# Kernel tuning notes

Measured on AMD Instinct MI355X. Metric: run time of the kernel, lower is better.

Reference implementation:

```python
import jax, jax.numpy as jnp
import numpy as np

ALPHA = 0.2  # LeakyReLU negative slope
NEG = -1e11  # mask value from original code (-100000000000.0)


def _gat_layer(x, adj_mask, W, av1, av2):
    # x: [N, F_in], W: [F_out, F_in], av1/av2: [F_out]
    wh = x @ W.T                                   # [N, F_out]
    wh1 = wh @ av1                                 # [N]
    wh2 = wh @ av2                                 # [N]
    e = wh1[:, None] + wh2[None, :]                # [N, N]
    e = jnp.where(e > 0, e, ALPHA * e)             # LeakyReLU
    att = jnp.where(adj_mask, e, NEG)
    att = jax.nn.softmax(att, axis=-1)
    return att @ wh                                # [N, F_out]


def setup_inputs() -> dict:
    key = jax.random.key(0)
    ks = jax.random.split(key, 8)
    N, F_IN, H, HID, NCLS = 4096, 512, 8, 64, 64
    s = 0.05  # xavier-ish scale
    x = jax.random.normal(ks[0], (N, F_IN), dtype=jnp.float32)
    adj = jax.random.randint(ks[1], (N, N), 0, 2, dtype=jnp.int32)
    W = jax.random.normal(ks[2], (H, HID, F_IN), dtype=jnp.float32) * s
    a1 = jax.random.normal(ks[3], (H, HID), dtype=jnp.float32) * s
    a2 = jax.random.normal(ks[4], (H, HID), dtype=jnp.float32) * s
    W2 = jax.random.normal(ks[5], (NCLS, H * HID), dtype=jnp.float32) * s
    a21 = jax.random.normal(ks[6], (NCLS,), dtype=jnp.float32) * s
    a22 = jax.random.normal(ks[7], (NCLS,), dtype=jnp.float32) * s
    return {"x": x, "adj": adj, "W": W, "a1": a1, "a2": a2,
            "W2": W2, "a21": a21, "a22": a22}


def reference(x, adj, W, a1, a2, W2, a21, a22):
    adj_mask = adj > 0                              # [N, N] bool
    # multi-head layers (concat=True -> ELU per head, concat on feature dim)
    heads = jax.vmap(_gat_layer, in_axes=(None, None, 0, 0, 0))(
        x, adj_mask, W, a1, a2)                     # [H, N, HID]
    heads = jax.nn.elu(heads)
    N = x.shape[0]
    h = jnp.transpose(heads, (1, 0, 2)).reshape(N, -1)  # [N, H*HID]
    # last layer (concat=False), then outer ELU + log_softmax
    out = _gat_layer(h, adj_mask, W2, a21, a22)     # [N, NCLS]
    out = jax.nn.elu(out)
    return jax.nn.log_softmax(out, axis=1)
```

## Files before the change

kernel.cpp:

```cpp
#include <hip/hip_runtime.h>

#define Nn 4096
#define FIN 512
#define NH 8
#define O1 512
#define LOG2E 1.44269504088896f

typedef __attribute__((ext_vector_type(8))) _Float16 half8;
typedef __attribute__((ext_vector_type(2))) _Float16 h2;
typedef __attribute__((ext_vector_type(4))) float f32x4;
typedef __attribute__((ext_vector_type(2))) unsigned int u32x2;
typedef unsigned long long ull;

__device__ __forceinline__ unsigned short f2bf(float f){
  union{float f; unsigned u;} x; x.f=f;
  unsigned r = x.u + 0x7fffu + ((x.u>>16)&1u);
  return (unsigned short)(r>>16);
}
__device__ __forceinline__ float bf2f(unsigned short b){
  union{unsigned u; float f;} x; x.u=((unsigned)b)<<16;
  return x.f;
}
__device__ __forceinline__ h2 pkrtz(float a, float b){
  return __builtin_bit_cast(h2, __builtin_amdgcn_cvt_pkrtz(a, b));
}
__device__ __forceinline__ h2 pkmul(h2 a, h2 b){
  h2 r; asm("v_pk_mul_f16 %0,%1,%2":"=v"(r):"v"(a),"v"(b)); return r;
}
__device__ __forceinline__ h2 pkmax(h2 a, h2 b){
  h2 r; asm("v_pk_max_f16 %0,%1,%2":"=v"(r):"v"(a),"v"(b)); return r;
}
__device__ __forceinline__ unsigned pairmask(unsigned bits, int k){
  unsigned s = ((bits >> (2*k)) * 0x8001u) & 0x10001u;
  return s * 0xFFFFu;
}
__device__ __forceinline__ void gload_lds16(const unsigned short* g, unsigned short* l){
  __builtin_amdgcn_global_load_lds(
      (const __attribute__((address_space(1))) unsigned int*)g,
      (__attribute__((address_space(3))) unsigned int*)l, 16, 0, 0);
}

__global__ void k_pack_adj(const int* __restrict__ adj, ull* __restrict__ adjw){
  const size_t total = (size_t)Nn*Nn;
  const size_t stride = (size_t)gridDim.x*blockDim.x;
  for (size_t tid = (size_t)blockIdx.x*blockDim.x + threadIdx.x; tid < total; tid += stride){
    int v = __builtin_nontemporal_load(adj + tid);
    ull m = __ballot(v>0);
    if((threadIdx.x&63)==0) adjw[tid>>6] = m;
  }
}

__global__ void k_cvt_all(const float* __restrict__ x, const float* __restrict__ W,
                          const float* __restrict__ W2,
                          unsigned short* __restrict__ xb, unsigned short* __restrict__ Wb,
                          unsigned short* __restrict__ W2b){
  const int NX = Nn*FIN, NW = O1*FIN, NW2 = 64*FIN;
  int i = (blockIdx.x*blockDim.x + threadIdx.x)*4;
  const float* src; unsigned short* dst; int off;
  if (i < NX){ src=x; dst=xb; off=i; }
  else if (i < NX+NW){ src=W; dst=Wb; off=i-NX; }
  else if (i < NX+NW+NW2){ src=W2; dst=W2b; off=i-NX-NW; }
  else return;
  float4 v = *(const float4*)(src+off);
  h2 lo = pkrtz(v.x, v.y);
  h2 hi = pkrtz(v.z, v.w);
  u32x2 pk; pk.x = __builtin_bit_cast(unsigned, lo); pk.y = __builtin_bit_cast(unsigned, hi);
  *(u32x2*)(dst+off) = pk;
}

template<int NWC, int KS>
__global__ __launch_bounds__(NWC*KS*64, 4)
void k_gemm3(const unsigned short* __restrict__ A, const unsigned short* __restrict__ B,
             unsigned short* __restrict__ CT, int M, int K, int O){
  int t=threadIdx.x, l=t&63, w=t>>6;
  int wc=w%NWC, ks=w/NWC;
  int m0=blockIdx.x*32, o0=blockIdx.y*(NWC*32);
  int row=l&15, kq=(l>>4)*8, g=l>>4;
  int kw=K/KS;
  const unsigned short* Ab = A + (size_t)(m0+row)*K + ks*kw + kq;
  const unsigned short* Bb = B + (size_t)(o0+wc*32+row)*K + ks*kw + kq;
  f32x4 acc[2][2]={};
  #pragma unroll 2
  for(int k0=0;k0<kw;k0+=32){
    half8 a0=*(const half8*)(Ab+k0);
    half8 a1=*(const half8*)(Ab+(size_t)16*K+k0);
    half8 b0=*(const half8*)(Bb+k0);
    half8 b1=*(const half8*)(Bb+(size_t)16*K+k0);
    acc[0][0]=__builtin_amdgcn_mfma_f32_16x16x32_f16(a0,b0,acc[0][0],0,0,0);
    acc[0][1]=__builtin_amdgcn_mfma_f32_16x16x32_f16(a0,b1,acc[0][1],0,0,0);
    acc[1][0]=__builtin_amdgcn_mfma_f32_16x16x32_f16(a1,b0,acc[1][0],0,0,0);
    acc[1][1]=__builtin_amdgcn_mfma_f32_16x16x32_f16(a1,b1,acc[1][1],0,0,0);
  }
  __shared__ float red[NWC][KS/2][32][36];
  for(int s=KS/2;s>=1;s>>=1){
    if(ks>=s && ks<2*s){
      #pragma unroll
      for(int mi=0;mi<2;mi++)
      #pragma unroll
      for(int oi=0;oi<2;oi++)
      #pragma unroll
      for(int r=0;r<4;r++)
        red[wc][ks-s][mi*16+g*4+r][oi*18+row]=acc[mi][oi][r];
    }
    __syncthreads();
    if(ks<s){
      #pragma unroll
      for(int mi=0;mi<2;mi++)
      #pragma unroll
      for(int oi=0;oi<2;oi++)
      #pragma unroll
      for(int r=0;r<4;r++)
        acc[mi][oi][r]+=red[wc][ks][mi*16+g*4+r][oi*18+row];
    }
    __syncthreads();
  }
  if(ks==0){
    #pragma unroll
    for(int mi=0;mi<2;mi++)
    #pragma unroll
    for(int oi=0;oi<2;oi++){
      int m=m0+mi*16+g*4;
      int o=o0+wc*32+oi*16+row;
      h2 lo = pkrtz(acc[mi][oi][0], acc[mi][oi][1]);
      h2 hi = pkrtz(acc[mi][oi][2], acc[mi][oi][3]);
      u32x2 pk; pk.x=__builtin_bit_cast(unsigned, lo); pk.y=__builtin_bit_cast(unsigned, hi);
      *(u32x2*)&CT[(size_t)o*M+m] = pk;
    }
  }
}

__global__ void k_wh12(const unsigned short* __restrict__ whT,
                       const float* __restrict__ a1, const float* __restrict__ a2,
                       float2* __restrict__ e1f1, unsigned short* __restrict__ E2a,
                       unsigned short* __restrict__ F2a){
  const int M=Nn;
  int n=blockIdx.x*blockDim.x+threadIdx.x;
  int h=blockIdx.y;
  float s1=0.f,s2=0.f;
  for(int c=0;c<64;c++){
    float v=(float)__builtin_bit_cast(_Float16, whT[(size_t)(h*64+c)*M+n]);
    s1+=v*a1[h*64+c];
    s2+=v*a2[h*64+c];
  }
  float s1L=s1*LOG2E, s2L=s2*LOG2E;
  float2 r1; r1.x=__builtin_amdgcn_exp2f(s1L); r1.y=__builtin_amdgcn_exp2f(0.2f*s1L);
  e1f1[(size_t)h*M+n]=r1;
  E2a[(size_t)h*M+n]=__builtin_bit_cast(unsigned short,(_Float16)__builtin_amdgcn_exp2f(s2L));
  F2a[(size_t)h*M+n]=__builtin_bit_cast(unsigned short,(_Float16)__builtin_amdgcn_exp2f(0.2f*s2L));
}

template<int JSTEPS, int LOGH, int JCLOG, int FINAL>
__global__ __launch_bounds__(256, 3)
void k_attn14(const ull* __restrict__ adjw,
              const float2* __restrict__ e1f1,
              const unsigned short* __restrict__ E2a,
              const unsigned short* __restrict__ F2a,
              const unsigned short* __restrict__ whT,
              unsigned short* __restrict__ Hmat,
              unsigned short* __restrict__ Opart, float* __restrict__ Dpart){
  const int M = Nn;
  __shared__ __align__(16) unsigned short vbuf[2][2][64][64];
  __shared__ __align__(16) unsigned short efbuf[2][2][JSTEPS*64];
  int t = threadIdx.x, l = t & 63, w = t >> 6;
  int rw = w & 1, jw = w >> 1;
  int lr = l & 15, g = l >> 4;
  int bid = blockIdx.x;
  int h = bid & ((1<<LOGH)-1);
  int bx = bid >> LOGH;
  int jc = bx & ((1<<JCLOG)-1);
  int rowtile = bx >> JCLOG;
  int i_base = rowtile*64 + rw*32;
  int jbase = jc*(2*JSTEPS*64) + jw*(JSTEPS*64);
  const unsigned short* Vb = whT + (size_t)h*64*M;

  h2 E1h[2], F1h[2];
  const ull *ar0, *ar1;
  {
    int i0 = i_base + lr, i1 = i_base + 16 + lr;
    float2 a = e1f1[(size_t)h*M + i0];
    float2 b = e1f1[(size_t)h*M + i1];
    E1h[0] = pkrtz(a.x, a.x);
    F1h[0] = pkrtz(a.y, a.y);
    E1h[1] = pkrtz(b.x, b.x);
    F1h[1] = pkrtz(b.y, b.y);
    ar0 = adjw + (size_t)i0*64 + (jbase>>6);
    ar1 = adjw + (size_t)i1*64 + (jbase>>6);
  }

  const unsigned short* vs[4];
  #pragma unroll
  for (int k=0;k<4;k++){
    int rloc = rw*32 + k*8 + (l>>3);
    vs[k] = Vb + (size_t)rloc*M + jbase + (((l&7)^(rloc&7))<<3);
  }

  {
    const unsigned short* src = (rw ? F2a : E2a) + (size_t)h*M + jbase;
    unsigned short* dst = &efbuf[jw][rw][0];
    constexpr int PB = JSTEPS*128;
    constexpr int NB = (PB + 1023)/1024;
    #pragma unroll
    for (int b=0;b<NB;b++){
      if (b*1024 + l*16 < PB)
        gload_lds16(src + b*512 + l*8, dst + b*512);
    }
  }

  half8 ones;
  #pragma unroll
  for (int q=0;q<8;q++) ones[q] = (_Float16)1.0f;

  f32x4 acc[2][4] = {};
  f32x4 accd[2] = {};

  #define STAGEV(slot, off) do{ \
      gload_lds16(vs[0] + (off)*64, &vbuf[jw][slot][rw*32   ][0]); \
      gload_lds16(vs[1] + (off)*64, &vbuf[jw][slot][rw*32+ 8][0]); \
      gload_lds16(vs[2] + (off)*64, &vbuf[jw][slot][rw*32+16][0]); \
      gload_lds16(vs[3] + (off)*64, &vbuf[jw][slot][rw*32+24][0]); \
    }while(0)

  STAGEV(0,0);
  ull w0 = ar0[0], w1 = ar1[0];
  asm volatile("s_waitcnt vmcnt(0)" ::: "memory");
  __builtin_amdgcn_sched_barrier(0);
  __builtin_amdgcn_s_barrier();

  const unsigned short* efE = &efbuf[jw][0][g*8];
  const unsigned short* efF = &efbuf[jw][1][g*8];

  for (int s0 = 0; s0 < JSTEPS; s0 += 4){
    #pragma unroll
    for (int u = 0; u < 4; u++){
      int s = s0 + u;
      ull wn0=0, wn1=0;
      if (s+1 < JSTEPS){
        wn0 = ar0[u+1]; wn1 = ar1[u+1];
        STAGEV((u+1)&1, u+1);
      }
      union { f32x4 f; h2 hh[4]; } Ee[2], Ff[2];
      #pragma unroll
      for (int half=0; half<2; half++){
        Ee[half].f = *(const f32x4*)(efE + u*64 + half*32);
        Ff[half].f = *(const f32x4*)(efF + u*64 + half*32);
      }
      unsigned pu[2][2][4];
      #pragma unroll
      for (int half=0; half<2; half++){
        unsigned bits0 = (unsigned)(w0 >> (half*32 + g*8)) & 0xffu;
        unsigned bits1 = (unsigned)(w1 >> (half*32 + g*8)) & 0xffu;
        #pragma unroll
        for (int k=0;k<4;k++){
          h2 e2 = Ee[half].hh[k], f2v = Ff[half].hh[k];
          h2 p0 = pkmax(pkmul(E1h[0], e2), pkmul(F1h[0], f2v));
          h2 p1 = pkmax(pkmul(E1h[1], e2), pkmul(F1h[1], f2v));
          pu[0][half][k] = __builtin_bit_cast(unsigned, p0) & pairmask(bits0,k);
          pu[1][half][k] = __builtin_bit_cast(unsigned, p1) & pairmask(bits1,k);
        }
      }
      __builtin_amdgcn_s_setprio(1);
      #pragma unroll
      for (int half=0; half<2; half++){
        half8 bfr[4];
        #pragma unroll
        for (int ct=0; ct<4; ct++)
          bfr[ct] = *(const half8*)&vbuf[jw][u&1][ct*16+lr][(((half*4+g)^(lr&7))<<3)];
        #pragma unroll
        for (int rf=0; rf<2; rf++){
          union { unsigned uu[4]; half8 v; } pv_;
          #pragma unroll
          for (int k=0;k<4;k++) pv_.uu[k] = pu[rf][half][k];
          #pragma unroll
          for (int ct=0; ct<4; ct++)
            acc[rf][ct] = __builtin_amdgcn_mfma_f32_16x16x32_f16(pv_.v, bfr[ct], acc[rf][ct], 0,0,0);
          accd[rf] = __builtin_amdgcn_mfma_f32_16x16x32_f16(pv_.v, ones, accd[rf], 0,0,0);
        }
      }
      __builtin_amdgcn_s_setprio(0);
      if (s+1 < JSTEPS){ w0 = wn0; w1 = wn1; }
      asm volatile("s_waitcnt vmcnt(0)" ::: "memory");
      __builtin_amdgcn_sched_barrier(0);
      __builtin_amdgcn_s_barrier();
    }
    #pragma unroll
    for (int k=0;k<4;k++) vs[k] += 256;
    ar0 += 4; ar1 += 4;
    efE += 256; efF += 256;
  }
  #undef STAGEV

  float* cmb  = (float*)&vbuf[0][0][0][0];
  float* cmbD = cmb + 64*65;
  __syncthreads();
  if (jw == 1){
    #pragma unroll
    for (int rf=0; rf<2; rf++){
      #pragma unroll
      for (int ct=0; ct<4; ct++)
        #pragma unroll
        for (int r=0; r<4; r++)
          cmb[(rw*32 + rf*16 + g*4 + r)*65 + ct*16 + lr] = acc[rf][ct][r];
      if (lr == 0){
        #pragma unroll
        for (int r=0; r<4; r++)
          cmbD[rw*32 + rf*16 + g*4 + r] = accd[rf][r];
      }
    }
  }
  __syncthreads();
  if (jw == 0){
    #pragma unroll
    for (int rf=0; rf<2; rf++){
      #pragma unroll
      for (int r=0; r<4; r++){
        int rloc = rw*32 + rf*16 + g*4 + r;
        float d = accd[rf][r] + cmbD[rloc];
        float rd = 1.f / fmaxf(d, 1e-30f);
        int row = rowtile*64 + rloc;
        if (FINAL){
          size_t pbase = (size_t)((h<<JCLOG)|jc)*Nn + row;
          if (lr == 0) Dpart[pbase] = d;
          #pragma unroll
          for (int ct=0; ct<4; ct++){
            float v = acc[rf][ct][r] + cmb[rloc*65 + ct*16 + lr];
            Opart[pbase*64 + ct*16 + lr] = f2bf(v);
          }
        } else {
          #pragma unroll
          for (int ct=0; ct<4; ct++){
            float v = (acc[rf][ct][r] + cmb[rloc*65 + ct*16 + lr]) * rd;
            v = v > 0.f ? v : __expf(v) - 1.f;
            Hmat[(size_t)row*O1 + h*64 + ct*16 + lr] =
                __builtin_bit_cast(unsigned short, (_Float16)v);
          }
        }
      }
    }
  }
}

__global__ void k_fin1(const unsigned short* __restrict__ Op, const float* __restrict__ Dp,
                       unsigned short* __restrict__ Hmat){
  int t = threadIdx.x;
  int c = t & 63, rr = t >> 6;
  int row = blockIdx.x*4 + rr, h = blockIdx.y;
  size_t b0 = (size_t)(h*2+0)*Nn + row;
  size_t b1 = (size_t)(h*2+1)*Nn + row;
  float o = bf2f(Op[b0*64+c]) + bf2f(Op[b1*64+c]);
  float d = Dp[b0] + Dp[b1];
  float v = o / fmaxf(d, 1e-30f);
  v = v > 0.f ? v : __expf(v) - 1.f;
  Hmat[(size_t)row*O1 + h*64 + c] = __builtin_bit_cast(unsigned short, (_Float16)v);
}

__global__ void k_fin2(const unsigned short* __restrict__ Op, const float* __restrict__ Dp,
                       float* __restrict__ out){
  int w = threadIdx.x>>6, l = threadIdx.x&63;
  int row = blockIdx.x*4 + w;
  float o = 0.f, d = 0.f;
  #pragma unroll
  for (int jc=0; jc<8; jc++){
    o += bf2f(Op[((size_t)jc*Nn + row)*64 + l]);
    d += Dp[(size_t)jc*Nn + row];
  }
  float v = o / fmaxf(d, 1e-30f);
  v = v > 0.f ? v : __expf(v) - 1.f;
  float m = v;
  #pragma unroll
  for (int dd=1; dd<64; dd<<=1) m = fmaxf(m, __shfl_xor(m, dd));
  float s = __expf(v - m);
  #pragma unroll
  for (int dd=1; dd<64; dd<<=1) s += __shfl_xor(s, dd);
  out[(size_t)row*64 + l] = v - (m + __logf(s));
}

extern "C" void kernel_launch(void* const* d_in, const int* in_sizes, int n_in,
                              void* d_out, int out_size, void* d_ws, size_t ws_size,
                              hipStream_t stream){
  const float* x  = (const float*)d_in[0];
  const int* adj  = (const int*)d_in[1];
  const float* W  = (const float*)d_in[2];
  const float* a1 = (const float*)d_in[3];
  const float* a2 = (const float*)d_in[4];
  const float* W2 = (const float*)d_in[5];
  const float* a21= (const float*)d_in[6];
  const float* a22= (const float*)d_in[7];
  float* out = (float*)d_out;
  char* ws = (char*)d_ws;

  size_t off=0;
  ull* adjw = (ull*)(ws+off); off += (size_t)Nn*64*8;
  unsigned short* xb   = (unsigned short*)(ws+off); off += (size_t)Nn*FIN*2;
  unsigned short* Wb   = (unsigned short*)(ws+off); off += (size_t)O1*FIN*2;
  unsigned short* W2b  = (unsigned short*)(ws+off); off += (size_t)64*FIN*2;
  unsigned short* whT1 = (unsigned short*)(ws+off); off += (size_t)O1*Nn*2;
  unsigned short* Hmat = (unsigned short*)(ws+off); off += (size_t)Nn*O1*2;
  unsigned short* whT2 = (unsigned short*)(ws+off); off += (size_t)64*Nn*2;
  float2* e1f1a = (float2*)(ws+off); off += (size_t)NH*Nn*8;
  unsigned short* E2aa = (unsigned short*)(ws+off); off += (size_t)NH*Nn*2;
  unsigned short* F2aa = (unsigned short*)(ws+off); off += (size_t)NH*Nn*2;
  float2* e1f1b = (float2*)(ws+off); off += (size_t)Nn*8;
  unsigned short* E2ab = (unsigned short*)(ws+off); off += (size_t)Nn*2;
  unsigned short* F2ab = (unsigned short*)(ws+off); off += (size_t)Nn*2;
  unsigned short* Opart = (unsigned short*)(ws+off); off += (size_t)16*Nn*64*2;
  float* Dpart = (float*)(ws+off); off += (size_t)16*Nn*4;

  k_pack_adj<<<2048, 256, 0, stream>>>(adj, adjw);
  {
    int tot = (Nn*FIN + O1*FIN + 64*FIN)/4;
    k_cvt_all<<<(tot+255)/256, 256, 0, stream>>>(x, W, W2, xb, Wb, W2b);
  }
  k_gemm3<2,4><<<dim3(Nn/32, O1/64), 512, 0, stream>>>(xb, Wb, whT1, Nn, FIN, O1);
  k_wh12<<<dim3(Nn/256, NH), 256, 0, stream>>>(whT1, a1, a2, e1f1a, E2aa, F2aa);
  k_attn14<16, 3, 1, 1><<<(Nn/64)*2*NH, 256, 0, stream>>>(adjw, e1f1a, E2aa, F2aa, whT1, nullptr, Opart, Dpart);
  k_fin1<<<dim3(Nn/4, NH), 256, 0, stream>>>(Opart, Dpart, Hmat);
  k_gemm3<1,8><<<dim3(Nn/32, 2), 512, 0, stream>>>(Hmat, W2b, whT2, Nn, FIN, 64);
  k_wh12<<<dim3(Nn/256, 1), 256, 0, stream>>>(whT2, a21, a22, e1f1b, E2ab, F2ab);
  k_attn14<4, 0, 3, 1><<<(Nn/64)*8, 256, 0, stream>>>(adjw, e1f1b, E2ab, F2ab, whT2, nullptr, Opart, Dpart);
  k_fin2<<<Nn/4, 256, 0, stream>>>(Opart, Dpart, out);
  (void)in_sizes; (void)n_in; (void)out_size; (void)ws_size;
}
```

Before: 116.7 us.

## Give each attention wave all 64 rows to double V-fragment reuse

The attention kernel now runs 2 waves per block instead of 4. Each wave covers all 64 query rows (4 row fragments) for its j-half, where before two waves each covered 32 rows. The aim is to halve LDS reads of the V fragments per MFMA and reduce per-block barrier overhead. The cost is more accumulator registers per wave (launch bounds cut to 2 blocks per CU of 128 threads), lower occupancy, and each wave now issues twice the V staging loads.

```diff
diff --git a/kernel.cpp b/kernel.cpp
--- a/kernel.cpp
+++ b/kernel.cpp
@@ -150,8 +150,8 @@
 }
 
 template<int JSTEPS, int LOGH, int JCLOG, int FINAL>
-__global__ __launch_bounds__(256, 3)
-void k_attn14(const ull* __restrict__ adjw,
+__global__ __launch_bounds__(128, 2)
+void k_attn15(const ull* __restrict__ adjw,
               const float2* __restrict__ e1f1,
               const unsigned short* __restrict__ E2a,
               const unsigned short* __restrict__ F2a,
@@ -161,48 +161,47 @@
   const int M = Nn;
   __shared__ __align__(16) unsigned short vbuf[2][2][64][64];
   __shared__ __align__(16) unsigned short efbuf[2][2][JSTEPS*64];
-  int t = threadIdx.x, l = t & 63, w = t >> 6;
-  int rw = w & 1, jw = w >> 1;
+  int t = threadIdx.x, l = t & 63, jw = t >> 6;
   int lr = l & 15, g = l >> 4;
   int bid = blockIdx.x;
   int h = bid & ((1<<LOGH)-1);
   int bx = bid >> LOGH;
   int jc = bx & ((1<<JCLOG)-1);
   int rowtile = bx >> JCLOG;
-  int i_base = rowtile*64 + rw*32;
+  int i_base = rowtile*64;
   int jbase = jc*(2*JSTEPS*64) + jw*(JSTEPS*64);
   const unsigned short* Vb = whT + (size_t)h*64*M;
 
-  h2 E1h[2], F1h[2];
-  const ull *ar0, *ar1;
+  h2 E1h[4], F1h[4];
+  const ull* ar[4];
+  #pragma unroll
+  for (int rf=0; rf<4; rf++){
+    int i = i_base + rf*16 + lr;
+    float2 a = e1f1[(size_t)h*M + i];
+    E1h[rf] = pkrtz(a.x, a.x);
+    F1h[rf] = pkrtz(a.y, a.y);
+    ar[rf] = adjw + (size_t)i*64 + (jbase>>6);
+  }
+
+  const unsigned short* vs[8];
+  #pragma unroll
+  for (int k=0;k<8;k++){
+    int rloc = k*8 + (l>>3);
+    vs[k] = Vb + (size_t)rloc*M + jbase + (((l&7)^(rloc&7))<<3);
+  }
+
   {
-    int i0 = i_base + lr, i1 = i_base + 16 + lr;
-    float2 a = e1f1[(size_t)h*M + i0];
-    float2 b = e1f1[(size_t)h*M + i1];
-    E1h[0] = pkrtz(a.x, a.x);
-    F1h[0] = pkrtz(a.y, a.y);
-    E1h[1] = pkrtz(b.x, b.x);
-    F1h[1] = pkrtz(b.y, b.y);
-    ar0 = adjw + (size_t)i0*64 + (jbase>>6);
-    ar1 = adjw + (size_t)i1*64 + (jbase>>6);
-  }
-
-  const unsigned short* vs[4];
-  #pragma unroll
-  for (int k=0;k<4;k++){
-    int rloc = rw*32 + k*8 + (l>>3);
-    vs[k] = Vb + (size_t)rloc*M + jbase + (((l&7)^(rloc&7))<<3);
-  }
-
-  {
-    const unsigned short* src = (rw ? F2a : E2a) + (size_t)h*M + jbase;
-    unsigned short* dst = &efbuf[jw][rw][0];
     constexpr int PB = JSTEPS*128;
     constexpr int NB = (PB + 1023)/1024;
     #pragma unroll
-    for (int b=0;b<NB;b++){
-      if (b*1024 + l*16 < PB)
-        gload_lds16(src + b*512 + l*8, dst + b*512);
+    for (int p=0;p<2;p++){
+      const unsigned short* src = (p ? F2a : E2a) + (size_t)h*M + jbase;
+      unsigned short* dst = &efbuf[jw][p][0];
+      #pragma unroll
+      for (int b=0;b<NB;b++){
+        if (b*1024 + l*16 < PB)
+          gload_lds16(src + b*512 + l*8, dst + b*512);
+      }
     }
   }
 
@@ -210,18 +209,24 @@
   #pragma unroll
   for (int q=0;q<8;q++) ones[q] = (_Float16)1.0f;
 
-  f32x4 acc[2][4] = {};
-  f32x4 accd[2] = {};
+  f32x4 acc[4][4] = {};
+  f32x4 accd[4] = {};
 
   #define STAGEV(slot, off) do{ \
-      gload_lds16(vs[0] + (off)*64, &vbuf[jw][slot][rw*32   ][0]); \
-      gload_lds16(vs[1] + (off)*64, &vbuf[jw][slot][rw*32+ 8][0]); \
-      gload_lds16(vs[2] + (off)*64, &vbuf[jw][slot][rw*32+16][0]); \
-      gload_lds16(vs[3] + (off)*64, &vbuf[jw][slot][rw*32+24][0]); \
+      gload_lds16(vs[0] + (off)*64, &vbuf[jw][slot][ 0][0]); \
+      gload_lds16(vs[1] + (off)*64, &vbuf[jw][slot][ 8][0]); \
+      gload_lds16(vs[2] + (off)*64, &vbuf[jw][slot][16][0]); \
+      gload_lds16(vs[3] + (off)*64, &vbuf[jw][slot][24][0]); \
+      gload_lds16(vs[4] + (off)*64, &vbuf[jw][slot][32][0]); \
+      gload_lds16(vs[5] + (off)*64, &vbuf[jw][slot][40][0]); \
+      gload_lds16(vs[6] + (off)*64, &vbuf[jw][slot][48][0]); \
+      gload_lds16(vs[7] + (off)*64, &vbuf[jw][slot][56][0]); \
     }while(0)
 
   STAGEV(0,0);
-  ull w0 = ar0[0], w1 = ar1[0];
+  ull w0[4];
+  #pragma unroll
+  for (int rf=0; rf<4; rf++) w0[rf] = ar[rf][0];
   asm volatile("s_waitcnt vmcnt(0)" ::: "memory");
   __builtin_amdgcn_sched_barrier(0);
   __builtin_amdgcn_s_barrier();
@@ -233,9 +238,10 @@
     #pragma unroll
     for (int u = 0; u < 4; u++){
       int s = s0 + u;
-      ull wn0=0, wn1=0;
+      ull wn[4] = {};
       if (s+1 < JSTEPS){
-        wn0 = ar0[u+1]; wn1 = ar1[u+1];
+        #pragma unroll
+        for (int rf=0; rf<4; rf++) wn[rf] = ar[rf][u+1];
         STAGEV((u+1)&1, u+1);
       }
       union { f32x4 f; h2 hh[4]; } Ee[2], Ff[2];
@@ -244,18 +250,20 @@
         Ee[half].f = *(const f32x4*)(efE + u*64 + half*32);
         Ff[half].f = *(const f32x4*)(efF + u*64 + half*32);
       }
-      unsigned pu[2][2][4];
+      unsigned pu[4][2][4];
       #pragma unroll
       for (int half=0; half<2; half++){
-        unsigned bits0 = (unsigned)(w0 >> (half*32 + g*8)) & 0xffu;
-        unsigned bits1 = (unsigned)(w1 >> (half*32 + g*8)) & 0xffu;
+        unsigned bits[4];
+        #pragma unroll
+        for (int rf=0; rf<4; rf++) bits[rf] = (unsigned)(w0[rf] >> (half*32 + g*8)) & 0xffu;
         #pragma unroll
         for (int k=0;k<4;k++){
           h2 e2 = Ee[half].hh[k], f2v = Ff[half].hh[k];
-          h2 p0 = pkmax(pkmul(E1h[0], e2), pkmul(F1h[0], f2v));
-          h2 p1 = pkmax(pkmul(E1h[1], e2), pkmul(F1h[1], f2v));
-          pu[0][half][k] = __builtin_bit_cast(unsigned, p0) & pairmask(bits0,k);
-          pu[1][half][k] = __builtin_bit_cast(unsigned, p1) & pairmask(bits1,k);
+          #pragma unroll
+          for (int rf=0; rf<4; rf++){
+            h2 p = pkmax(pkmul(E1h[rf], e2), pkmul(F1h[rf], f2v));
+            pu[rf][half][k] = __builtin_bit_cast(unsigned, p) & pairmask(bits[rf],k);
+          }
         }
       }
       __builtin_amdgcn_s_setprio(1);
@@ -266,7 +274,7 @@
         for (int ct=0; ct<4; ct++)
           bfr[ct] = *(const half8*)&vbuf[jw][u&1][ct*16+lr][(((half*4+g)^(lr&7))<<3)];
         #pragma unroll
-        for (int rf=0; rf<2; rf++){
+        for (int rf=0; rf<4; rf++){
           union { unsigned uu[4]; half8 v; } pv_;
           #pragma unroll
           for (int k=0;k<4;k++) pv_.uu[k] = pu[rf][half][k];
@@ -277,14 +285,18 @@
         }
       }
       __builtin_amdgcn_s_setprio(0);
-      if (s+1 < JSTEPS){ w0 = wn0; w1 = wn1; }
+      if (s+1 < JSTEPS){
+        #pragma unroll
+        for (int rf=0; rf<4; rf++) w0[rf] = wn[rf];
+      }
       asm volatile("s_waitcnt vmcnt(0)" ::: "memory");
       __builtin_amdgcn_sched_barrier(0);
       __builtin_amdgcn_s_barrier();
     }
     #pragma unroll
-    for (int k=0;k<4;k++) vs[k] += 256;
-    ar0 += 4; ar1 += 4;
+    for (int k=0;k<8;k++) vs[k] += 256;
+    #pragma unroll
+    for (int rf=0; rf<4; rf++) ar[rf] += 4;
     efE += 256; efF += 256;
   }
   #undef STAGEV
@@ -294,26 +306,26 @@
   __syncthreads();
   if (jw == 1){
     #pragma unroll
-    for (int rf=0; rf<2; rf++){
+    for (int rf=0; rf<4; rf++){
       #pragma unroll
       for (int ct=0; ct<4; ct++)
         #pragma unroll
         for (int r=0; r<4; r++)
-          cmb[(rw*32 + rf*16 + g*4 + r)*65 + ct*16 + lr] = acc[rf][ct][r];
+          cmb[(rf*16 + g*4 + r)*65 + ct*16 + lr] = acc[rf][ct][r];
       if (lr == 0){
         #pragma unroll
         for (int r=0; r<4; r++)
-          cmbD[rw*32 + rf*16 + g*4 + r] = accd[rf][r];
+          cmbD[rf*16 + g*4 + r] = accd[rf][r];
       }
     }
   }
   __syncthreads();
   if (jw == 0){
     #pragma unroll
-    for (int rf=0; rf<2; rf++){
+    for (int rf=0; rf<4; rf++){
       #pragma unroll
       for (int r=0; r<4; r++){
-        int rloc = rw*32 + rf*16 + g*4 + r;
+        int rloc = rf*16 + g*4 + r;
         float d = accd[rf][r] + cmbD[rloc];
         float rd = 1.f / fmaxf(d, 1e-30f);
         int row = rowtile*64 + rloc;
@@ -412,11 +424,11 @@
   }
   k_gemm3<2,4><<<dim3(Nn/32, O1/64), 512, 0, stream>>>(xb, Wb, whT1, Nn, FIN, O1);
   k_wh12<<<dim3(Nn/256, NH), 256, 0, stream>>>(whT1, a1, a2, e1f1a, E2aa, F2aa);
-  k_attn14<16, 3, 1, 1><<<(Nn/64)*2*NH, 256, 0, stream>>>(adjw, e1f1a, E2aa, F2aa, whT1, nullptr, Opart, Dpart);
+  k_attn15<16, 3, 1, 1><<<(Nn/64)*2*NH, 128, 0, stream>>>(adjw, e1f1a, E2aa, F2aa, whT1, nullptr, Opart, Dpart);
   k_fin1<<<dim3(Nn/4, NH), 256, 0, stream>>>(Opart, Dpart, Hmat);
   k_gemm3<1,8><<<dim3(Nn/32, 2), 512, 0, stream>>>(Hmat, W2b, whT2, Nn, FIN, 64);
   k_wh12<<<dim3(Nn/256, 1), 256, 0, stream>>>(whT2, a21, a22, e1f1b, E2ab, F2ab);
-  k_attn14<4, 0, 3, 1><<<(Nn/64)*8, 256, 0, stream>>>(adjw, e1f1b, E2ab, F2ab, whT2, nullptr, Opart, Dpart);
+  k_attn15<4, 0, 3, 1><<<(Nn/64)*8, 128, 0, stream>>>(adjw, e1f1b, E2ab, F2ab, whT2, nullptr, Opart, Dpart);
   k_fin2<<<Nn/4, 256, 0, stream>>>(Opart, Dpart, out);
   (void)in_sizes; (void)n_in; (void)out_size; (void)ws_size;
 }
```

After: 127.7 us. 9.4% more time.
